# Kernel tuning notes

Hardware: AMD Instinct MI355X
Metric: run time of the kernel (lower is better)

## Reference

```python
import jax, jax.numpy as jnp
import numpy as np

B, T, N = 32, 128, 30
D_T, D_V, D_I = 512, 512, 512


def setup_inputs() -> dict:
    key = jax.random.key(0)
    ks = jax.random.split(key, 9)
    return {
        "h_s": jax.random.normal(ks[0], (B, N, D_T), dtype=jnp.float32),
        "h_v": jax.random.normal(ks[1], (B, T, D_V), dtype=jnp.float32),
        "lengths": jax.random.randint(ks[2], (B,), 1, N + 1, dtype=jnp.int32),
        "W_S": jax.random.normal(ks[3], (D_T, D_I), dtype=jnp.float32) * 0.05,
        "b_S": jax.random.normal(ks[4], (D_I,), dtype=jnp.float32) * 0.05,
        "W_V": jax.random.normal(ks[5], (D_V, D_I), dtype=jnp.float32) * 0.05,
        "b_V": jax.random.normal(ks[6], (D_I,), dtype=jnp.float32) * 0.05,
        "W_w": jax.random.normal(ks[7], (D_I,), dtype=jnp.float32) * 0.05,
        "b_w": jax.random.normal(ks[8], (1,), dtype=jnp.float32) * 0.05,
    }


def reference(h_s, h_v, lengths, W_S, b_S, W_V, b_V, W_w, b_w):
    n_tok = h_s.shape[1]
    # token mask (B, N): 1 where position < length
    mask = (lengths[:, None] >= jnp.arange(1, n_tok + 1)[None, :]).astype(h_s.dtype)
    # loop-invariant projections computed once (the torch loop recomputes per t)
    S = h_s @ W_S + b_S                      # (B, N, D_I)
    V = h_v @ W_V + b_V                      # (B, T, D_I)
    # additive attention scores beta: (B, T, N)
    e = jnp.tanh(S[:, None, :, :] + V[:, :, None, :])  # (B, T, N, D_I)
    beta = jnp.einsum('btnd,d->btn', e, W_w) + b_w[0]
    # masked softmax (non-memory-efficient variant, faithful to source)
    m = mask[:, None, :]                      # (B, 1, N)
    p = jax.nn.softmax(beta * m, axis=-1) * m
    alpha = p / (p.sum(axis=-1, keepdims=True) + 1e-13) + 1e-13  # (B, T, N)
    # attended textual features: (B, T, D_T)
    return jnp.einsum('btn,bnd->btd', alpha, h_s)
```

## Files before the change

kernel.cpp:

```cpp
#include <hip/hip_runtime.h>
#include <math.h>

#define BB 32
#define TT 128
#define NTOK 30
#define DD 512
#define C2F 2.885390081777927f

typedef unsigned short u16;
typedef __attribute__((ext_vector_type(8))) short bf16x8;
typedef __attribute__((ext_vector_type(8))) unsigned short u16x8;
typedef __attribute__((ext_vector_type(4))) float f32x4;

__device__ __forceinline__ u16 f2bf(float f) {
    unsigned u = __builtin_bit_cast(unsigned, f);
    u += 0x7fffu + ((u >> 16) & 1u);
    return (u16)(u >> 16);
}
__device__ __forceinline__ float bf2f(u16 u) {
    return __builtin_bit_cast(float, (unsigned)u << 16);
}

__device__ __forceinline__ void load_lds16(const u16* g, u16* l) {
    __builtin_amdgcn_global_load_lds(
        (const __attribute__((address_space(1))) unsigned int*)g,
        (__attribute__((address_space(3))) unsigned int*)l,
        16, 0, 0);
}

template<int CTRL>
__device__ __forceinline__ float dpp_add(float x) {
    int yi = __builtin_amdgcn_update_dpp(0, __builtin_bit_cast(int, x), CTRL, 0xF, 0xF, true);
    return x + __builtin_bit_cast(float, yi);
}
__device__ __forceinline__ float red64(float x) {
    x = dpp_add<0xB1>(x);
    x = dpp_add<0x4E>(x);
    x = dpp_add<0x141>(x);
    x = dpp_add<0x140>(x);
    x += __shfl_xor(x, 16, 64);
    x += __shfl_xor(x, 32, 64);
    return x;
}

__global__ __launch_bounds__(256) void prep(
    const float* __restrict__ W_S, const float* __restrict__ W_V,
    u16* __restrict__ WtS, u16* __restrict__ WtV)
{
    __shared__ u16 tile[32][33];
    int idx = blockIdx.x;
    const float* W = (idx & 256) ? W_V : W_S;
    u16*        T  = (idx & 256) ? WtV : WtS;
    idx &= 255;
    int k0 = (idx >> 4) * 32, n0 = (idx & 15) * 32;
    int c = threadIdx.x & 31, r8 = threadIdx.x >> 5;
    #pragma unroll
    for (int q = 0; q < 4; ++q) {
        int k = r8 + q * 8;
        tile[k][c] = f2bf(W[(size_t)(k0 + k) * DD + n0 + c]);
    }
    __syncthreads();
    #pragma unroll
    for (int q = 0; q < 4; ++q) {
        int n = r8 + q * 8;
        T[(size_t)(n0 + n) * DD + k0 + c] = tile[c][n];
    }
}

__global__ __launch_bounds__(256) void gemm_mfma(
    const float* __restrict__ h_s, const float* __restrict__ h_v,
    const u16* __restrict__ WtS, const u16* __restrict__ WtV,
    const float* __restrict__ b_S, const float* __restrict__ b_V,
    u16* __restrict__ Sbf, u16* __restrict__ Vbf)
{
    __shared__ u16 ldsA[64 * 64];
    __shared__ u16 ldsB[64 * 64];
    const int bid = blockIdx.x;
    const int by  = bid & 7;
    const int bxx = bid >> 3;
    const float* A; const u16* Bt; const float* bias; u16* Y; int bm;
    if (bxx < 15) { A = h_s; Bt = WtS; bias = b_S; Y = Sbf; bm = bxx * 64; }
    else          { A = h_v; Bt = WtV; bias = b_V; Y = Vbf; bm = (bxx - 15) * 64; }
    const int bn = by * 64;

    const int tid  = threadIdx.x;
    const int lane = tid & 63;
    const int wid  = tid >> 6;
    const int wr = wid >> 1, wc = wid & 1;

    const int rowA0 = tid >> 3,          chA0 = tid & 7;
    const int rowA1 = (tid + 256) >> 3,  chA1 = tid & 7;
    const float* gA0 = A + (size_t)(bm + rowA0) * DD + chA0 * 8;
    const float* gA1 = A + (size_t)(bm + rowA1) * DD + chA1 * 8;
    u16* wA0 = ldsA + rowA0 * 64 + ((chA0 ^ (rowA0 & 7)) * 8);
    u16* wA1 = ldsA + rowA1 * 64 + ((chA1 ^ (rowA1 & 7)) * 8);

    const int idx0 = tid,       rowB0 = idx0 >> 3, chB0 = (idx0 & 7) ^ (rowB0 & 7);
    const int idx1 = 256 + tid, rowB1 = idx1 >> 3, chB1 = (idx1 & 7) ^ (rowB1 & 7);
    const u16* gB0 = Bt + (size_t)(bn + rowB0) * DD + chB0 * 8;
    const u16* gB1 = Bt + (size_t)(bn + rowB1) * DD + chB1 * 8;
    u16* lB0 = ldsB + wid * 512;
    u16* lB1 = ldsB + 2048 + wid * 512;

    const int arow = wr * 32 + (lane & 15);
    const int brow = wc * 32 + (lane & 15);
    const int kq   = lane >> 4;
    const int sw   = lane & 7;

    f32x4 acc[2][2];
    #pragma unroll
    for (int i = 0; i < 2; ++i)
        #pragma unroll
        for (int j = 0; j < 2; ++j)
            acc[i][j] = (f32x4){0.f, 0.f, 0.f, 0.f};

    for (int k0 = 0; k0 < DD; k0 += 64) {
        float4 a00 = *(const float4*)(gA0 + k0);
        float4 a01 = *(const float4*)(gA0 + k0 + 4);
        float4 a10 = *(const float4*)(gA1 + k0);
        float4 a11 = *(const float4*)(gA1 + k0 + 4);
        __syncthreads();
        bf16x8 p0, p1;
        p0[0]=(short)f2bf(a00.x); p0[1]=(short)f2bf(a00.y); p0[2]=(short)f2bf(a00.z); p0[3]=(short)f2bf(a00.w);
        p0[4]=(short)f2bf(a01.x); p0[5]=(short)f2bf(a01.y); p0[6]=(short)f2bf(a01.z); p0[7]=(short)f2bf(a01.w);
        p1[0]=(short)f2bf(a10.x); p1[1]=(short)f2bf(a10.y); p1[2]=(short)f2bf(a10.z); p1[3]=(short)f2bf(a10.w);
        p1[4]=(short)f2bf(a11.x); p1[5]=(short)f2bf(a11.y); p1[6]=(short)f2bf(a11.z); p1[7]=(short)f2bf(a11.w);
        *(bf16x8*)wA0 = p0;
        *(bf16x8*)wA1 = p1;
        load_lds16(gB0 + k0, lB0);
        load_lds16(gB1 + k0, lB1);
        __syncthreads();

        bf16x8 af[2][2], bfr[2][2];
        #pragma unroll
        for (int i = 0; i < 2; ++i)
            #pragma unroll
            for (int s = 0; s < 2; ++s) {
                int ra = arow + i * 16;
                af[i][s]  = *(const bf16x8*)(ldsA + ra * 64 + ((s * 4 + kq) ^ sw) * 8);
                int rb = brow + i * 16;
                bfr[i][s] = *(const bf16x8*)(ldsB + rb * 64 + ((s * 4 + kq) ^ sw) * 8);
            }
        #pragma unroll
        for (int s = 0; s < 2; ++s)
            #pragma unroll
            for (int i = 0; i < 2; ++i)
                #pragma unroll
                for (int j = 0; j < 2; ++j)
                    acc[i][j] = __builtin_amdgcn_mfma_f32_16x16x32_bf16(
                        af[i][s], bfr[j][s], acc[i][j], 0, 0, 0);
    }

    #pragma unroll
    for (int i = 0; i < 2; ++i)
        #pragma unroll
        for (int j = 0; j < 2; ++j) {
            int r = bm + wr * 32 + i * 16 + (lane >> 4) * 4;
            int c = bn + wc * 32 + j * 16 + (lane & 15);
            float bv = bias[c];
            #pragma unroll
            for (int reg = 0; reg < 4; ++reg)
                Y[(size_t)(r + reg) * DD + c] = f2bf((acc[i][j][reg] + bv) * C2F);
        }
}

__global__ __launch_bounds__(512) void attend3(
    const u16* __restrict__ Sbf, const u16* __restrict__ Vbf,
    const float* __restrict__ h_s, const int* __restrict__ lengths,
    const float* __restrict__ W_w, const float* __restrict__ b_w,
    float* __restrict__ out)
{
    __shared__ u16 Slds[NTOK * DD];
    const int b  = blockIdx.x >> 4;
    const int tc = blockIdx.x & 15;
    const int tid  = threadIdx.x;
    const int w    = tid >> 6;
    const int lane = tid & 63;
    const int t_glob = tc * 8 + w;
    const int len = lengths[b];
    const int d0 = lane * 8;
    const float bwv = b_w[0];

    {
        const uint4* src = (const uint4*)(Sbf + (size_t)b * NTOK * DD);
        uint4* dst = (uint4*)Slds;
        #pragma unroll
        for (int i = 0; i < 4; ++i) {
            int idx = i * 512 + tid;
            if (idx < NTOK * DD / 8) dst[idx] = src[idx];
        }
    }

    float v[8], ww[8];
    {
        u16x8 v8 = *(const u16x8*)(Vbf + ((size_t)(b * TT + t_glob)) * DD + d0);
        float4 w0 = *(const float4*)&W_w[d0];
        float4 w1 = *(const float4*)&W_w[d0 + 4];
        #pragma unroll
        for (int j = 0; j < 8; ++j) v[j] = bf2f(v8[j]);
        ww[0]=w0.x; ww[1]=w0.y; ww[2]=w0.z; ww[3]=w0.w;
        ww[4]=w1.x; ww[5]=w1.y; ww[6]=w1.z; ww[7]=w1.w;
    }
    float wpart = 0.f;
    #pragma unroll
    for (int j = 0; j < 8; ++j) wpart += ww[j];
    const float wsum = red64(wpart);

    __syncthreads();

    float pacc[NTOK];
    #pragma unroll
    for (int n = 0; n < NTOK; ++n) {
        u16x8 s8 = *(const u16x8*)(Slds + n * DD + d0);
        float a = 0.f;
        #pragma unroll
        for (int j = 0; j < 8; ++j) {
            float e = __builtin_amdgcn_exp2f(bf2f(s8[j]) + v[j]);
            a = fmaf(ww[j], __builtin_amdgcn_rcpf(1.f + e), a);
        }
        pacc[n] = red64(a);
    }
    __syncthreads();

    float mx = -1e30f;
    #pragma unroll
    for (int n = 0; n < NTOK; ++n) {
        float bn = fmaf(-2.f, pacc[n], wsum + bwv);
        pacc[n] = bn;
        if (n < len) mx = fmaxf(mx, bn);
    }
    float ssum = 0.f;
    #pragma unroll
    for (int n = 0; n < NTOK; ++n) {
        float e = (n < len) ? __expf(pacc[n] - mx) : 0.f;
        pacc[n] = e;
        ssum += e;
    }
    const float inv = 1.f / (ssum + 1e-13f);
    #pragma unroll
    for (int n = 0; n < NTOK; ++n) pacc[n] = fmaf(pacc[n], inv, 1e-13f);

    {
        const float4* src = (const float4*)(h_s + (size_t)b * NTOK * DD);
        ushort4* dst = (ushort4*)Slds;
        #pragma unroll
        for (int i = 0; i < 8; ++i) {
            int idx = i * 512 + tid;
            if (idx < NTOK * DD / 4) {
                float4 hv = src[idx];
                ushort4 pk;
                pk.x = f2bf(hv.x); pk.y = f2bf(hv.y);
                pk.z = f2bf(hv.z); pk.w = f2bf(hv.w);
                dst[idx] = pk;
            }
        }
    }
    __syncthreads();

    float acc8[8] = {};
    #pragma unroll
    for (int n = 0; n < NTOK; ++n) {
        float a = pacc[n];
        u16x8 h8 = *(const u16x8*)(Slds + n * DD + d0);
        #pragma unroll
        for (int j = 0; j < 8; ++j)
            acc8[j] = fmaf(a, bf2f(h8[j]), acc8[j]);
    }
    float* Or = out + ((size_t)(b * TT + t_glob)) * DD + d0;
    *(float4*)&Or[0] = make_float4(acc8[0], acc8[1], acc8[2], acc8[3]);
    *(float4*)&Or[4] = make_float4(acc8[4], acc8[5], acc8[6], acc8[7]);
}

extern "C" void kernel_launch(void* const* d_in, const int* in_sizes, int n_in,
                              void* d_out, int out_size, void* d_ws, size_t ws_size,
                              hipStream_t stream) {
    const float* h_s     = (const float*)d_in[0];
    const float* h_v     = (const float*)d_in[1];
    const int*   lengths = (const int*)  d_in[2];
    const float* W_S     = (const float*)d_in[3];
    const float* b_S     = (const float*)d_in[4];
    const float* W_V     = (const float*)d_in[5];
    const float* b_V     = (const float*)d_in[6];
    const float* W_w     = (const float*)d_in[7];
    const float* b_w     = (const float*)d_in[8];
    float* out = (float*)d_out;

    u16* Sbf = (u16*)d_ws;
    u16* Vbf = Sbf + (size_t)BB * NTOK * DD;
    u16* WtS = Vbf + (size_t)BB * TT * DD;
    u16* WtV = WtS + (size_t)DD * DD;

    prep<<<512, 256, 0, stream>>>(W_S, W_V, WtS, WtV);
    gemm_mfma<<<(15 + 64) * 8, 256, 0, stream>>>(
        h_s, h_v, WtS, WtV, b_S, b_V, Sbf, Vbf);
    attend3<<<BB * 16, 512, 0, stream>>>(Sbf, Vbf, h_s, lengths, W_w, b_w, out);
}
```

Baseline: 50.63 us.

## Pre-convert GEMM activations to bf16 and load A tiles via direct-to-LDS

Adds a conversion pass in the prep kernel that writes h_s and h_v as bf16 into workspace. The GEMM then streams A tiles with global_load_lds like the B tiles, dropping the fp32 loads and per-element conversions from its inner loop. The GEMM grid is also remapped into groups of 8 row tiles by 8 column tiles for better L2 reuse, with padded blocks exiting early. The cost is an extra read and write of the activations in a separate pass, plus more workspace.

```diff
diff --git a/kernel.cpp b/kernel.cpp
--- a/kernel.cpp
+++ b/kernel.cpp
@@ -43,12 +43,28 @@
     return x;
 }
 
+#define NCONV ((BB*NTOK*DD + BB*TT*DD)/4/256)
 __global__ __launch_bounds__(256) void prep(
+    const float* __restrict__ h_s, const float* __restrict__ h_v,
     const float* __restrict__ W_S, const float* __restrict__ W_V,
+    u16* __restrict__ Abf_s, u16* __restrict__ Abf_v,
     u16* __restrict__ WtS, u16* __restrict__ WtV)
 {
     __shared__ u16 tile[32][33];
-    int idx = blockIdx.x;
+    int bx = blockIdx.x;
+    if (bx < NCONV) {
+        int i = bx * 256 + threadIdx.x;
+        const int n0_4 = BB * NTOK * DD / 4;
+        const float* x; u16* y;
+        if (i < n0_4) { x = h_s; y = Abf_s; }
+        else { i -= n0_4; x = h_v; y = Abf_v; }
+        float4 v = ((const float4*)x)[i];
+        ushort4 o;
+        o.x = f2bf(v.x); o.y = f2bf(v.y); o.z = f2bf(v.z); o.w = f2bf(v.w);
+        ((ushort4*)y)[i] = o;
+        return;
+    }
+    int idx = bx - NCONV;
     const float* W = (idx & 256) ? W_V : W_S;
     u16*        T  = (idx & 256) ? WtV : WtS;
     idx &= 255;
@@ -68,7 +84,7 @@
 }
 
 __global__ __launch_bounds__(256) void gemm_mfma(
-    const float* __restrict__ h_s, const float* __restrict__ h_v,
+    const u16* __restrict__ Abf_s, const u16* __restrict__ Abf_v,
     const u16* __restrict__ WtS, const u16* __restrict__ WtV,
     const float* __restrict__ b_S, const float* __restrict__ b_V,
     u16* __restrict__ Sbf, u16* __restrict__ Vbf)
@@ -76,11 +92,13 @@
     __shared__ u16 ldsA[64 * 64];
     __shared__ u16 ldsB[64 * 64];
     const int bid = blockIdx.x;
-    const int by  = bid & 7;
-    const int bxx = bid >> 3;
-    const float* A; const u16* Bt; const float* bias; u16* Y; int bm;
-    if (bxx < 15) { A = h_s; Bt = WtS; bias = b_S; Y = Sbf; bm = bxx * 64; }
-    else          { A = h_v; Bt = WtV; bias = b_V; Y = Vbf; bm = (bxx - 15) * 64; }
+    const int grp = bid >> 6, rem = bid & 63;
+    const int by  = rem >> 3;
+    const int bxx = grp * 8 + (rem & 7);
+    if (bxx >= 15 + 64) return;
+    const u16* A; const u16* Bt; const float* bias; u16* Y; int bm;
+    if (bxx < 15) { A = Abf_s; Bt = WtS; bias = b_S; Y = Sbf; bm = bxx * 64; }
+    else          { A = Abf_v; Bt = WtV; bias = b_V; Y = Vbf; bm = (bxx - 15) * 64; }
     const int bn = by * 64;
 
     const int tid  = threadIdx.x;
@@ -88,17 +106,14 @@
     const int wid  = tid >> 6;
     const int wr = wid >> 1, wc = wid & 1;
 
-    const int rowA0 = tid >> 3,          chA0 = tid & 7;
-    const int rowA1 = (tid + 256) >> 3,  chA1 = tid & 7;
-    const float* gA0 = A + (size_t)(bm + rowA0) * DD + chA0 * 8;
-    const float* gA1 = A + (size_t)(bm + rowA1) * DD + chA1 * 8;
-    u16* wA0 = ldsA + rowA0 * 64 + ((chA0 ^ (rowA0 & 7)) * 8);
-    u16* wA1 = ldsA + rowA1 * 64 + ((chA1 ^ (rowA1 & 7)) * 8);
-
-    const int idx0 = tid,       rowB0 = idx0 >> 3, chB0 = (idx0 & 7) ^ (rowB0 & 7);
-    const int idx1 = 256 + tid, rowB1 = idx1 >> 3, chB1 = (idx1 & 7) ^ (rowB1 & 7);
-    const u16* gB0 = Bt + (size_t)(bn + rowB0) * DD + chB0 * 8;
-    const u16* gB1 = Bt + (size_t)(bn + rowB1) * DD + chB1 * 8;
+    const int idx0 = tid,       row0 = idx0 >> 3, ch0 = (idx0 & 7) ^ (row0 & 7);
+    const int idx1 = 256 + tid, row1 = idx1 >> 3, ch1 = (idx1 & 7) ^ (row1 & 7);
+    const u16* gA0 = A  + (size_t)(bm + row0) * DD + ch0 * 8;
+    const u16* gA1 = A  + (size_t)(bm + row1) * DD + ch1 * 8;
+    const u16* gB0 = Bt + (size_t)(bn + row0) * DD + ch0 * 8;
+    const u16* gB1 = Bt + (size_t)(bn + row1) * DD + ch1 * 8;
+    u16* lA0 = ldsA + wid * 512;
+    u16* lA1 = ldsA + 2048 + wid * 512;
     u16* lB0 = ldsB + wid * 512;
     u16* lB1 = ldsB + 2048 + wid * 512;
 
@@ -115,18 +130,9 @@
             acc[i][j] = (f32x4){0.f, 0.f, 0.f, 0.f};
 
     for (int k0 = 0; k0 < DD; k0 += 64) {
-        float4 a00 = *(const float4*)(gA0 + k0);
-        float4 a01 = *(const float4*)(gA0 + k0 + 4);
-        float4 a10 = *(const float4*)(gA1 + k0);
-        float4 a11 = *(const float4*)(gA1 + k0 + 4);
         __syncthreads();
-        bf16x8 p0, p1;
-        p0[0]=(short)f2bf(a00.x); p0[1]=(short)f2bf(a00.y); p0[2]=(short)f2bf(a00.z); p0[3]=(short)f2bf(a00.w);
-        p0[4]=(short)f2bf(a01.x); p0[5]=(short)f2bf(a01.y); p0[6]=(short)f2bf(a01.z); p0[7]=(short)f2bf(a01.w);
-        p1[0]=(short)f2bf(a10.x); p1[1]=(short)f2bf(a10.y); p1[2]=(short)f2bf(a10.z); p1[3]=(short)f2bf(a10.w);
-        p1[4]=(short)f2bf(a11.x); p1[5]=(short)f2bf(a11.y); p1[6]=(short)f2bf(a11.z); p1[7]=(short)f2bf(a11.w);
-        *(bf16x8*)wA0 = p0;
-        *(bf16x8*)wA1 = p1;
+        load_lds16(gA0 + k0, lA0);
+        load_lds16(gA1 + k0, lA1);
         load_lds16(gB0 + k0, lB0);
         load_lds16(gB1 + k0, lB1);
         __syncthreads();
@@ -285,13 +291,15 @@
     const float* b_w     = (const float*)d_in[8];
     float* out = (float*)d_out;
 
-    u16* Sbf = (u16*)d_ws;
-    u16* Vbf = Sbf + (size_t)BB * NTOK * DD;
-    u16* WtS = Vbf + (size_t)BB * TT * DD;
-    u16* WtV = WtS + (size_t)DD * DD;
-
-    prep<<<512, 256, 0, stream>>>(W_S, W_V, WtS, WtV);
-    gemm_mfma<<<(15 + 64) * 8, 256, 0, stream>>>(
-        h_s, h_v, WtS, WtV, b_S, b_V, Sbf, Vbf);
+    u16* Sbf   = (u16*)d_ws;
+    u16* Vbf   = Sbf + (size_t)BB * NTOK * DD;
+    u16* WtS   = Vbf + (size_t)BB * TT * DD;
+    u16* WtV   = WtS + (size_t)DD * DD;
+    u16* Abf_s = WtV + (size_t)DD * DD;
+    u16* Abf_v = Abf_s + (size_t)BB * NTOK * DD;
+
+    prep<<<NCONV + 512, 256, 0, stream>>>(h_s, h_v, W_S, W_V, Abf_s, Abf_v, WtS, WtV);
+    gemm_mfma<<<640, 256, 0, stream>>>(
+        Abf_s, Abf_v, WtS, WtV, b_S, b_V, Sbf, Vbf);
     attend3<<<BB * 16, 512, 0, stream>>>(Sbf, Vbf, h_s, lengths, W_w, b_w, out);
 }
```

Result: faster. 42.55 us (-16.0%).

## Double-buffer GEMM tiles, grid-swizzle blocks, export bf16 h_s for attention stage

Applied to the files above, without the earlier changes.

The projection GEMM moves to 512 threads with 8 waves (each wave covers a 32x16 output slice) and double-buffered LDS. The next K-tile's global loads are issued before the MFMAs on the current tile, and one barrier per iteration is dropped. Blocks are regrouped so eight M-tiles share each N column, and the by==0 blocks also write the bf16-converted h_s to workspace. The attention kernel then loads both S and bf16 h_s into separate LDS arrays up front, which removes the second fp32 conversion pass and two barriers at the cost of doubling LDS per block (about 60KB), which may reduce occupancy.

```diff
diff --git a/kernel.cpp b/kernel.cpp
--- a/kernel.cpp
+++ b/kernel.cpp
@@ -67,110 +67,103 @@
     }
 }
 
-__global__ __launch_bounds__(256) void gemm_mfma(
+__global__ __launch_bounds__(512) void gemm_mfma(
     const float* __restrict__ h_s, const float* __restrict__ h_v,
     const u16* __restrict__ WtS, const u16* __restrict__ WtV,
     const float* __restrict__ b_S, const float* __restrict__ b_V,
-    u16* __restrict__ Sbf, u16* __restrict__ Vbf)
+    u16* __restrict__ Sbf, u16* __restrict__ Vbf, u16* __restrict__ Abf_s)
 {
-    __shared__ u16 ldsA[64 * 64];
-    __shared__ u16 ldsB[64 * 64];
+    __shared__ u16 ldsA[2][64 * 64];
+    __shared__ u16 ldsB[2][64 * 64];
     const int bid = blockIdx.x;
-    const int by  = bid & 7;
-    const int bxx = bid >> 3;
+    const int grp = bid >> 6, rem = bid & 63;
+    const int by  = rem >> 3;
+    const int bxx = grp * 8 + (rem & 7);
+    if (bxx >= 15 + 64) return;
     const float* A; const u16* Bt; const float* bias; u16* Y; int bm;
     if (bxx < 15) { A = h_s; Bt = WtS; bias = b_S; Y = Sbf; bm = bxx * 64; }
     else          { A = h_v; Bt = WtV; bias = b_V; Y = Vbf; bm = (bxx - 15) * 64; }
     const int bn = by * 64;
+    const bool wrA = (bxx < 15) && (by == 0);
 
     const int tid  = threadIdx.x;
     const int lane = tid & 63;
     const int wid  = tid >> 6;
-    const int wr = wid >> 1, wc = wid & 1;
-
-    const int rowA0 = tid >> 3,          chA0 = tid & 7;
-    const int rowA1 = (tid + 256) >> 3,  chA1 = tid & 7;
-    const float* gA0 = A + (size_t)(bm + rowA0) * DD + chA0 * 8;
-    const float* gA1 = A + (size_t)(bm + rowA1) * DD + chA1 * 8;
-    u16* wA0 = ldsA + rowA0 * 64 + ((chA0 ^ (rowA0 & 7)) * 8);
-    u16* wA1 = ldsA + rowA1 * 64 + ((chA1 ^ (rowA1 & 7)) * 8);
-
-    const int idx0 = tid,       rowB0 = idx0 >> 3, chB0 = (idx0 & 7) ^ (rowB0 & 7);
-    const int idx1 = 256 + tid, rowB1 = idx1 >> 3, chB1 = (idx1 & 7) ^ (rowB1 & 7);
-    const u16* gB0 = Bt + (size_t)(bn + rowB0) * DD + chB0 * 8;
-    const u16* gB1 = Bt + (size_t)(bn + rowB1) * DD + chB1 * 8;
-    u16* lB0 = ldsB + wid * 512;
-    u16* lB1 = ldsB + 2048 + wid * 512;
+    const int wr = wid >> 2, wc = wid & 3;
+
+    const int srow = tid >> 3, slc = tid & 7;
+    const int ssc  = slc ^ (srow & 7);
+    const float* gA = A + (size_t)(bm + srow) * DD + slc * 8;
+    const u16*   gB = Bt + (size_t)(bn + srow) * DD + ssc * 8;
+    u16* wAp[2] = { &ldsA[0][srow * 64 + ssc * 8], &ldsA[1][srow * 64 + ssc * 8] };
+    u16* wBp[2] = { &ldsB[0][wid * 512],           &ldsB[1][wid * 512] };
+    u16* expA = Abf_s + (size_t)(bm + srow) * DD + slc * 8;
 
     const int arow = wr * 32 + (lane & 15);
-    const int brow = wc * 32 + (lane & 15);
+    const int brow = wc * 16 + (lane & 15);
     const int kq   = lane >> 4;
     const int sw   = lane & 7;
 
-    f32x4 acc[2][2];
-    #pragma unroll
-    for (int i = 0; i < 2; ++i)
-        #pragma unroll
-        for (int j = 0; j < 2; ++j)
-            acc[i][j] = (f32x4){0.f, 0.f, 0.f, 0.f};
-
-    for (int k0 = 0; k0 < DD; k0 += 64) {
-        float4 a00 = *(const float4*)(gA0 + k0);
-        float4 a01 = *(const float4*)(gA0 + k0 + 4);
-        float4 a10 = *(const float4*)(gA1 + k0);
-        float4 a11 = *(const float4*)(gA1 + k0 + 4);
+    f32x4 acc[2];
+    acc[0] = (f32x4){0.f, 0.f, 0.f, 0.f};
+    acc[1] = (f32x4){0.f, 0.f, 0.f, 0.f};
+
+    float4 a0 = *(const float4*)(gA);
+    float4 a1 = *(const float4*)(gA + 4);
+    load_lds16(gB, wBp[0]);
+
+    for (int t = 0; t < 8; ++t) {
+        const int cur = t & 1;
+        bf16x8 p;
+        p[0]=(short)f2bf(a0.x); p[1]=(short)f2bf(a0.y); p[2]=(short)f2bf(a0.z); p[3]=(short)f2bf(a0.w);
+        p[4]=(short)f2bf(a1.x); p[5]=(short)f2bf(a1.y); p[6]=(short)f2bf(a1.z); p[7]=(short)f2bf(a1.w);
+        *(bf16x8*)wAp[cur] = p;
+        if (wrA) *(bf16x8*)(expA + t * 64) = p;
+
         __syncthreads();
-        bf16x8 p0, p1;
-        p0[0]=(short)f2bf(a00.x); p0[1]=(short)f2bf(a00.y); p0[2]=(short)f2bf(a00.z); p0[3]=(short)f2bf(a00.w);
-        p0[4]=(short)f2bf(a01.x); p0[5]=(short)f2bf(a01.y); p0[6]=(short)f2bf(a01.z); p0[7]=(short)f2bf(a01.w);
-        p1[0]=(short)f2bf(a10.x); p1[1]=(short)f2bf(a10.y); p1[2]=(short)f2bf(a10.z); p1[3]=(short)f2bf(a10.w);
-        p1[4]=(short)f2bf(a11.x); p1[5]=(short)f2bf(a11.y); p1[6]=(short)f2bf(a11.z); p1[7]=(short)f2bf(a11.w);
-        *(bf16x8*)wA0 = p0;
-        *(bf16x8*)wA1 = p1;
-        load_lds16(gB0 + k0, lB0);
-        load_lds16(gB1 + k0, lB1);
-        __syncthreads();
-
-        bf16x8 af[2][2], bfr[2][2];
-        #pragma unroll
-        for (int i = 0; i < 2; ++i)
+
+        if (t < 7) {
+            a0 = *(const float4*)(gA + (t + 1) * 64);
+            a1 = *(const float4*)(gA + (t + 1) * 64 + 4);
+            load_lds16(gB + (t + 1) * 64, wBp[cur ^ 1]);
+        }
+
+        bf16x8 af[2][2], bf[2];
+        #pragma unroll
+        for (int s = 0; s < 2; ++s) {
             #pragma unroll
-            for (int s = 0; s < 2; ++s) {
+            for (int i = 0; i < 2; ++i) {
                 int ra = arow + i * 16;
-                af[i][s]  = *(const bf16x8*)(ldsA + ra * 64 + ((s * 4 + kq) ^ sw) * 8);
-                int rb = brow + i * 16;
-                bfr[i][s] = *(const bf16x8*)(ldsB + rb * 64 + ((s * 4 + kq) ^ sw) * 8);
+                af[i][s] = *(const bf16x8*)(&ldsA[cur][ra * 64 + ((s * 4 + kq) ^ sw) * 8]);
             }
+            bf[s] = *(const bf16x8*)(&ldsB[cur][brow * 64 + ((s * 4 + kq) ^ sw) * 8]);
+        }
         #pragma unroll
         for (int s = 0; s < 2; ++s)
             #pragma unroll
             for (int i = 0; i < 2; ++i)
-                #pragma unroll
-                for (int j = 0; j < 2; ++j)
-                    acc[i][j] = __builtin_amdgcn_mfma_f32_16x16x32_bf16(
-                        af[i][s], bfr[j][s], acc[i][j], 0, 0, 0);
-    }
-
-    #pragma unroll
-    for (int i = 0; i < 2; ++i)
-        #pragma unroll
-        for (int j = 0; j < 2; ++j) {
-            int r = bm + wr * 32 + i * 16 + (lane >> 4) * 4;
-            int c = bn + wc * 32 + j * 16 + (lane & 15);
-            float bv = bias[c];
-            #pragma unroll
-            for (int reg = 0; reg < 4; ++reg)
-                Y[(size_t)(r + reg) * DD + c] = f2bf((acc[i][j][reg] + bv) * C2F);
-        }
-}
-
-__global__ __launch_bounds__(512) void attend3(
+                acc[i] = __builtin_amdgcn_mfma_f32_16x16x32_bf16(af[i][s], bf[s], acc[i], 0, 0, 0);
+    }
+
+    #pragma unroll
+    for (int i = 0; i < 2; ++i) {
+        int r = bm + wr * 32 + i * 16 + (lane >> 4) * 4;
+        int c = bn + wc * 16 + (lane & 15);
+        float bv = bias[c];
+        #pragma unroll
+        for (int reg = 0; reg < 4; ++reg)
+            Y[(size_t)(r + reg) * DD + c] = f2bf((acc[i][reg] + bv) * C2F);
+    }
+}
+
+__global__ __launch_bounds__(512) void attend4(
     const u16* __restrict__ Sbf, const u16* __restrict__ Vbf,
-    const float* __restrict__ h_s, const int* __restrict__ lengths,
+    const u16* __restrict__ Hbf, const int* __restrict__ lengths,
     const float* __restrict__ W_w, const float* __restrict__ b_w,
     float* __restrict__ out)
 {
-    __shared__ u16 Slds[NTOK * DD];
+    __shared__ u16 Sl[NTOK * DD];
+    __shared__ u16 Hl[NTOK * DD];
     const int b  = blockIdx.x >> 4;
     const int tc = blockIdx.x & 15;
     const int tid  = threadIdx.x;
@@ -182,12 +175,14 @@
     const float bwv = b_w[0];
 
     {
-        const uint4* src = (const uint4*)(Sbf + (size_t)b * NTOK * DD);
-        uint4* dst = (uint4*)Slds;
+        const uint4* sS = (const uint4*)(Sbf + (size_t)b * NTOK * DD);
+        const uint4* sH = (const uint4*)(Hbf + (size_t)b * NTOK * DD);
+        uint4* dS = (uint4*)Sl;
+        uint4* dH = (uint4*)Hl;
         #pragma unroll
         for (int i = 0; i < 4; ++i) {
             int idx = i * 512 + tid;
-            if (idx < NTOK * DD / 8) dst[idx] = src[idx];
+            if (idx < NTOK * DD / 8) { dS[idx] = sS[idx]; dH[idx] = sH[idx]; }
         }
     }
 
@@ -211,7 +206,7 @@
     float pacc[NTOK];
     #pragma unroll
     for (int n = 0; n < NTOK; ++n) {
-        u16x8 s8 = *(const u16x8*)(Slds + n * DD + d0);
+        u16x8 s8 = *(const u16x8*)(Sl + n * DD + d0);
         float a = 0.f;
         #pragma unroll
         for (int j = 0; j < 8; ++j) {
@@ -220,7 +215,6 @@
         }
         pacc[n] = red64(a);
     }
-    __syncthreads();
 
     float mx = -1e30f;
     #pragma unroll
@@ -240,28 +234,11 @@
     #pragma unroll
     for (int n = 0; n < NTOK; ++n) pacc[n] = fmaf(pacc[n], inv, 1e-13f);
 
-    {
-        const float4* src = (const float4*)(h_s + (size_t)b * NTOK * DD);
-        ushort4* dst = (ushort4*)Slds;
-        #pragma unroll
-        for (int i = 0; i < 8; ++i) {
-            int idx = i * 512 + tid;
-            if (idx < NTOK * DD / 4) {
-                float4 hv = src[idx];
-                ushort4 pk;
-                pk.x = f2bf(hv.x); pk.y = f2bf(hv.y);
-                pk.z = f2bf(hv.z); pk.w = f2bf(hv.w);
-                dst[idx] = pk;
-            }
-        }
-    }
-    __syncthreads();
-
     float acc8[8] = {};
     #pragma unroll
     for (int n = 0; n < NTOK; ++n) {
         float a = pacc[n];
-        u16x8 h8 = *(const u16x8*)(Slds + n * DD + d0);
+        u16x8 h8 = *(const u16x8*)(Hl + n * DD + d0);
         #pragma unroll
         for (int j = 0; j < 8; ++j)
             acc8[j] = fmaf(a, bf2f(h8[j]), acc8[j]);
@@ -285,13 +262,14 @@
     const float* b_w     = (const float*)d_in[8];
     float* out = (float*)d_out;
 
-    u16* Sbf = (u16*)d_ws;
-    u16* Vbf = Sbf + (size_t)BB * NTOK * DD;
-    u16* WtS = Vbf + (size_t)BB * TT * DD;
-    u16* WtV = WtS + (size_t)DD * DD;
+    u16* Sbf   = (u16*)d_ws;
+    u16* Vbf   = Sbf + (size_t)BB * NTOK * DD;
+    u16* WtS   = Vbf + (size_t)BB * TT * DD;
+    u16* WtV   = WtS + (size_t)DD * DD;
+    u16* Abf_s = WtV + (size_t)DD * DD;
 
     prep<<<512, 256, 0, stream>>>(W_S, W_V, WtS, WtV);
-    gemm_mfma<<<(15 + 64) * 8, 256, 0, stream>>>(
-        h_s, h_v, WtS, WtV, b_S, b_V, Sbf, Vbf);
-    attend3<<<BB * 16, 512, 0, stream>>>(Sbf, Vbf, h_s, lengths, W_w, b_w, out);
-}
+    gemm_mfma<<<640, 512, 0, stream>>>(
+        h_s, h_v, WtS, WtV, b_S, b_V, Sbf, Vbf, Abf_s);
+    attend4<<<BB * 16, 512, 0, stream>>>(Sbf, Vbf, Abf_s, lengths, W_w, b_w, out);
+}
```

New measurement: 46.89 us. 7.4% less time.
